# Kernel tuning notes

Measured on AMD Instinct MI355X. Metric: run time of the kernel, lower is better.

The kernel has to match this reference:

```python
import jax, jax.numpy as jnp
import numpy as np

N = 50000
E = 800000
NFEAT, NHID, NCLASS = 256, 128, 32


def setup_inputs() -> dict:
    key = jax.random.key(0)
    ks = jax.random.split(key, 8)
    x = jax.random.normal(ks[0], (N, NFEAT), dtype=jnp.float32)
    edge_src = jax.random.randint(ks[1], (E,), 0, N, dtype=jnp.int32)
    edge_dst = jax.random.randint(ks[2], (E,), 0, N, dtype=jnp.int32)
    edge_weight = jax.random.uniform(ks[3], (E,), dtype=jnp.float32)
    # Linear layer params (torch Linear: y = x @ W.T + b); store as [in, out]
    s1 = 1.0 / np.sqrt(NFEAT)
    s2 = 1.0 / np.sqrt(NHID)
    W1 = jax.random.uniform(ks[4], (NFEAT, NHID), jnp.float32, -s1, s1)
    b1 = jax.random.uniform(ks[5], (NHID,), jnp.float32, -s1, s1)
    W2 = jax.random.uniform(ks[6], (NHID, NCLASS), jnp.float32, -s2, s2)
    b2 = jax.random.uniform(ks[7], (NCLASS,), jnp.float32, -s2, s2)
    return {"x": x, "edge_src": edge_src, "edge_dst": edge_dst,
            "edge_weight": edge_weight, "W1": W1, "b1": b1, "W2": W2, "b2": b2}


def spmm(edge_src, edge_dst, edge_weight, h):
    # out[dst] += w * h[src]  -- sparse adjacency @ dense features
    msgs = edge_weight[:, None] * h[edge_src]          # [E, F]
    return jax.ops.segment_sum(msgs, edge_dst, num_segments=N)


def reference(x, edge_src, edge_dst, edge_weight, W1, b1, W2, b2):
    # GCN layer 1: Linear -> SpMM -> ReLU (dropout inactive in eval mode)
    h = x @ W1 + b1                                    # [N, NHID]
    h = spmm(edge_src, edge_dst, edge_weight, h)
    h = jax.nn.relu(h)
    # GCN layer 2: Linear -> SpMM
    h = h @ W2 + b2                                    # [N, NCLASS]
    out = spmm(edge_src, edge_dst, edge_weight, h)
    return out
```

## Files before the change

### kernel.cpp

```cpp
#include <hip/hip_runtime.h>

#define NFEAT 256
#define NHID 128
#define NCLASS 32

typedef __attribute__((ext_vector_type(8))) short short8;
typedef __attribute__((ext_vector_type(4))) float f32x4;
typedef __attribute__((ext_vector_type(4))) int int4v;

static __device__ __forceinline__ unsigned short f2bf(float f) {
    unsigned u = __float_as_uint(f);
    unsigned r = (u + 0x7fffu + ((u >> 16) & 1u)) >> 16;
    return (unsigned short)r;
}
static __device__ __forceinline__ float bf_lo(unsigned d) {
    return __uint_as_float(d << 16);
}
static __device__ __forceinline__ float bf_hi(unsigned d) {
    return __uint_as_float(d & 0xffff0000u);
}

__global__ __launch_bounds__(256) void prep_kernel(
    const float* __restrict__ W1, unsigned short* __restrict__ W1t,
    const int* __restrict__ dst, int* __restrict__ bkt_partial,
    int E, int CE, int shift)
{
    const int tid = threadIdx.x;
    if (blockIdx.x < 128) {
        int o = blockIdx.x * 256 + tid;
        int c = o >> 8, k = o & 255;
        W1t[o] = f2bf(W1[(size_t)k * NHID + c]);
    } else {
        __shared__ int h[256];
        const int kb = blockIdx.x - 128;
        const int start = kb * CE;
        const int end = min(start + CE, E);
        h[tid] = 0;
        __syncthreads();
        for (int e = start + tid; e < end; e += 256)
            atomicAdd(&h[dst[e] >> shift], 1);
        __syncthreads();
        bkt_partial[kb * 256 + tid] = h[tid];
    }
}

__global__ __launch_bounds__(256) void scan_kernel(
    const int* __restrict__ bkt_partial, int* __restrict__ chunk_pre,
    int* __restrict__ bkt_base, int E)
{
    __shared__ int s[256];
    const int t = threadIdx.x;
    int run = 0;
    for (int kb = 0; kb < 256; ++kb) {
        chunk_pre[kb * 256 + t] = run;
        run += bkt_partial[kb * 256 + t];
    }
    s[t] = run;
    __syncthreads();
    for (int off = 1; off < 256; off <<= 1) {
        int tv = (t >= off) ? s[t - off] : 0;
        __syncthreads();
        s[t] += tv;
        __syncthreads();
    }
    bkt_base[t] = s[t] - run;
    if (t == 255) bkt_base[256] = s[255];
}

__global__ __launch_bounds__(256) void bucket_scatter_kernel(
    const int* __restrict__ src, const int* __restrict__ dst,
    const float* __restrict__ w, const int* __restrict__ bkt_base,
    const int* __restrict__ chunk_pre, uint2* __restrict__ bkt_edges,
    int E, int CE, int shift)
{
    __shared__ int cur[256];
    const int tid = threadIdx.x;
    const int kb = blockIdx.x;
    cur[tid] = bkt_base[tid] + chunk_pre[kb * 256 + tid];
    __syncthreads();
    const int start = kb * CE;
    const int end = min(start + CE, E);
    const unsigned lmask = (1u << shift) - 1u;
    for (int e = start + tid; e < end; e += 256) {
        int d = dst[e];
        int b = d >> shift;
        int pos = atomicAdd(&cur[b], 1);
        uint2 rec;
        rec.x = (unsigned)src[e] | (((unsigned)d & lmask) << 24);
        rec.y = __float_as_uint(w[e]);
        bkt_edges[pos] = rec;
    }
}

__global__ __launch_bounds__(1024) void fine_scatter_kernel(
    const int* __restrict__ bkt_base, const uint2* __restrict__ bkt_edges,
    int* __restrict__ row_ptr, uint2* __restrict__ csr_e,
    int shift, int N, int E)
{
    __shared__ int h[256];
    __shared__ int cur[256];
    const int b = blockIdx.x;
    const int t = threadIdx.x;
    const int lo = bkt_base[b], hi = bkt_base[b + 1];
    const int dbase = b << shift;

    if (t < 256) h[t] = 0;
    __syncthreads();
    for (int i = lo + t; i < hi; i += 1024)
        atomicAdd(&h[bkt_edges[i].x >> 24], 1);
    __syncthreads();
    int v = (t < 256) ? h[t] : 0;
    for (int off = 1; off < 256; off <<= 1) {
        int tv = (t >= off && t < 256) ? h[t - off] : 0;
        __syncthreads();
        if (t < 256) h[t] += tv;
        __syncthreads();
    }
    if (t < 256) {
        int excl = h[t] - v;
        int r = dbase + t;
        if (r < N) row_ptr[r] = lo + excl;
        cur[t] = lo + excl;
    }
    if (b == 0 && t == 0) row_ptr[N] = E;
    __syncthreads();
    for (int i = lo + t; i < hi; i += 1024) {
        uint2 rec = bkt_edges[i];
        int dl = rec.x >> 24;
        int pos = atomicAdd(&cur[dl], 1);
        uint2 o;
        o.x = rec.x & 0xFFFFFFu;
        o.y = rec.y;
        csr_e[pos] = o;
    }
}

__global__ __launch_bounds__(256) void gemm1_mfma_kernel(
    const float* __restrict__ x, const unsigned short* __restrict__ W1t,
    const float* __restrict__ b1, unsigned short* __restrict__ h1b, int N)
{
    __shared__ unsigned short wt[128 * 256];
    __shared__ unsigned short xs[64 * 64];

    const int tid = threadIdx.x;
    const int lane = tid & 63;
    const int wv = tid >> 6;
    const int row0 = blockIdx.x * 64;
    const int l15 = lane & 15;
    const int l47 = lane >> 4;
    const int r7 = lane & 7;

    {
        const int4v* src = (const int4v*)W1t;
#pragma unroll
        for (int j = 0; j < 16; ++j) {
            int si = tid + j * 256;
            int c = si >> 5, s = si & 31;
            int sp = (s & 24) | ((s & 7) ^ (c & 7));
            int4v v = src[si];
            *(int4v*)&wt[c * 256 + sp * 8] = v;
        }
    }

    auto stage_x = [&](int t) {
#pragma unroll
        for (int j = 0; j < 2; ++j) {
            int si = tid + j * 256;
            int r = si >> 3, s = si & 7;
            int row = row0 + r;
            float4 v0 = make_float4(0.f, 0.f, 0.f, 0.f), v1 = v0;
            if (row < N) {
                const float4* xp = (const float4*)&x[(size_t)row * NFEAT + t * 64 + s * 8];
                v0 = xp[0]; v1 = xp[1];
            }
            int w0 = f2bf(v0.x) | ((unsigned)f2bf(v0.y) << 16);
            int w1 = f2bf(v0.z) | ((unsigned)f2bf(v0.w) << 16);
            int w2 = f2bf(v1.x) | ((unsigned)f2bf(v1.y) << 16);
            int w3 = f2bf(v1.z) | ((unsigned)f2bf(v1.w) << 16);
            int sp = s ^ (r & 7);
            int4v pv; pv[0] = w0; pv[1] = w1; pv[2] = w2; pv[3] = w3;
            *(int4v*)&xs[r * 64 + sp * 8] = pv;
        }
    };

    f32x4 acc[8];
#pragma unroll
    for (int cf = 0; cf < 8; ++cf)
#pragma unroll
        for (int r = 0; r < 4; ++r) acc[cf][r] = 0.f;

    stage_x(0);
    __syncthreads();

    const int arow = wv * 16 + l15;
#pragma unroll
    for (int t = 0; t < 4; ++t) {
        short8 af[2];
#pragma unroll
        for (int kf = 0; kf < 2; ++kf) {
            int slot = (kf * 4 + l47) ^ r7;
            af[kf] = *(const short8*)&xs[arow * 64 + slot * 8];
        }
#pragma unroll
        for (int cf = 0; cf < 8; ++cf) {
            const int brow = cf * 16 + l15;
#pragma unroll
            for (int kf = 0; kf < 2; ++kf) {
                int slot = t * 8 + ((kf * 4 + l47) ^ r7);
                short8 bfr = *(const short8*)&wt[brow * 256 + slot * 8];
                acc[cf] = __builtin_amdgcn_mfma_f32_16x16x32_bf16(af[kf], bfr, acc[cf], 0, 0, 0);
            }
        }
        __syncthreads();
        if (t < 3) {
            stage_x(t + 1);
            __syncthreads();
        }
    }

#pragma unroll
    for (int cf = 0; cf < 8; ++cf) {
        float bias = b1[cf * 16 + l15];
#pragma unroll
        for (int r = 0; r < 4; ++r) {
            int row = row0 + wv * 16 + l47 * 4 + r;
            if (row < N)
                h1b[(size_t)row * NHID + cf * 16 + l15] = f2bf(acc[cf][r] + bias);
        }
    }
}

__global__ __launch_bounds__(512) void spmm1_gemm2_kernel(
    const int* __restrict__ row_ptr, const uint2* __restrict__ csr_e,
    const unsigned short* __restrict__ h1b, const float* __restrict__ W2,
    const float* __restrict__ b2, unsigned* __restrict__ h2b, int N)
{
    __shared__ float w2s[NHID * NCLASS];
    __shared__ float hrow[8][NHID];
    const int tid = threadIdx.x;
#pragma unroll
    for (int j = 0; j < 8; ++j) {
        int idx = tid + j * 512;
        w2s[idx] = W2[idx];
    }
    __syncthreads();

    const int lane = tid & 63;
    const int wv = tid >> 6;
    const int row = __builtin_amdgcn_readfirstlane(blockIdx.x * 8 + wv);
    if (row >= N) return;

    const int e0 = row_ptr[row], e1 = row_ptr[row + 1];
    const size_t loff = (size_t)(lane * 2);
    float a0 = 0.f, a1 = 0.f;
    int e = e0;
    for (; e + 8 <= e1; e += 8) {
        uint2 r[8];
#pragma unroll
        for (int j = 0; j < 8; ++j) r[j] = csr_e[e + j];
        unsigned d[8];
#pragma unroll
        for (int j = 0; j < 8; ++j)
            d[j] = *(const unsigned*)(h1b + (size_t)r[j].x * NHID + loff);
#pragma unroll
        for (int j = 0; j < 8; ++j) {
            float w = __uint_as_float(r[j].y);
            a0 += w * bf_lo(d[j]); a1 += w * bf_hi(d[j]);
        }
    }
    if (e + 4 <= e1) {
        uint2 r[4];
#pragma unroll
        for (int j = 0; j < 4; ++j) r[j] = csr_e[e + j];
        unsigned d[4];
#pragma unroll
        for (int j = 0; j < 4; ++j)
            d[j] = *(const unsigned*)(h1b + (size_t)r[j].x * NHID + loff);
#pragma unroll
        for (int j = 0; j < 4; ++j) {
            float w = __uint_as_float(r[j].y);
            a0 += w * bf_lo(d[j]); a1 += w * bf_hi(d[j]);
        }
        e += 4;
    }
    if (e + 2 <= e1) {
        uint2 r0 = csr_e[e], r1 = csr_e[e + 1];
        unsigned d0 = *(const unsigned*)(h1b + (size_t)r0.x * NHID + loff);
        unsigned d1 = *(const unsigned*)(h1b + (size_t)r1.x * NHID + loff);
        float w0 = __uint_as_float(r0.y), w1 = __uint_as_float(r1.y);
        a0 += w0 * bf_lo(d0); a1 += w0 * bf_hi(d0);
        a0 += w1 * bf_lo(d1); a1 += w1 * bf_hi(d1);
        e += 2;
    }
    if (e < e1) {
        uint2 r = csr_e[e];
        float w = __uint_as_float(r.y);
        unsigned d = *(const unsigned*)(h1b + (size_t)r.x * NHID + loff);
        a0 += w * bf_lo(d); a1 += w * bf_hi(d);
    }
    *(float2*)&hrow[wv][lane * 2] = make_float2(fmaxf(a0, 0.f), fmaxf(a1, 0.f));

    const int c = lane & 31;
    const int kh = lane >> 5;
    const float* hw = &hrow[wv][kh * 64];
    const float* wp = &w2s[(size_t)kh * 64 * NCLASS + c];
    float acc = 0.f;
#pragma unroll
    for (int k = 0; k < 64; ++k)
        acc += hw[k] * wp[k * NCLASS];
    acc += __shfl(acc, lane ^ 32);
    float accb = acc + b2[c];
    float nb = __shfl(accb, lane ^ 1);
    if (kh == 0 && (lane & 1) == 0) {
        unsigned u = (unsigned)f2bf(accb) | ((unsigned)f2bf(nb) << 16);
        h2b[(size_t)row * 16 + (lane >> 1)] = u;
    }
}

__global__ __launch_bounds__(256) void spmm2_kernel(
    const int* __restrict__ row_ptr, const uint2* __restrict__ csr_e,
    const unsigned* __restrict__ h2b, float* __restrict__ out, int N)
{
    const int li = threadIdx.x & 15;
    const int g = threadIdx.x >> 4;
    const int row = blockIdx.x * 16 + g;
    if (row >= N) return;
    const int e0 = row_ptr[row], e1 = row_ptr[row + 1];
    float a0 = 0.f, a1 = 0.f;
    int e = e0;
    for (; e + 8 <= e1; e += 8) {
        uint2 r[8];
#pragma unroll
        for (int j = 0; j < 8; ++j) r[j] = csr_e[e + j];
        unsigned d[8];
#pragma unroll
        for (int j = 0; j < 8; ++j) d[j] = h2b[(size_t)r[j].x * 16 + li];
#pragma unroll
        for (int j = 0; j < 8; ++j) {
            float w = __uint_as_float(r[j].y);
            a0 += w * bf_lo(d[j]); a1 += w * bf_hi(d[j]);
        }
    }
    for (; e + 2 <= e1; e += 2) {
        uint2 r0 = csr_e[e], r1 = csr_e[e + 1];
        unsigned d0 = h2b[(size_t)r0.x * 16 + li];
        unsigned d1 = h2b[(size_t)r1.x * 16 + li];
        float w0 = __uint_as_float(r0.y), w1 = __uint_as_float(r1.y);
        a0 += w0 * bf_lo(d0); a1 += w0 * bf_hi(d0);
        a0 += w1 * bf_lo(d1); a1 += w1 * bf_hi(d1);
    }
    if (e < e1) {
        uint2 r = csr_e[e];
        float w = __uint_as_float(r.y);
        unsigned d = h2b[(size_t)r.x * 16 + li];
        a0 += w * bf_lo(d); a1 += w * bf_hi(d);
    }
    *(float2*)&out[(size_t)row * NCLASS + li * 2] = make_float2(a0, a1);
}


extern "C" void kernel_launch(void* const* d_in, const int* in_sizes, int n_in,
                              void* d_out, int out_size, void* d_ws, size_t ws_size,
                              hipStream_t stream) {
    const float* x    = (const float*)d_in[0];
    const int*   esrc = (const int*)d_in[1];
    const int*   edst = (const int*)d_in[2];
    const float* ew   = (const float*)d_in[3];
    const float* W1   = (const float*)d_in[4];
    const float* b1   = (const float*)d_in[5];
    const float* W2   = (const float*)d_in[6];
    const float* b2   = (const float*)d_in[7];
    float* out = (float*)d_out;

    const int N = in_sizes[0] / NFEAT;
    const int E = in_sizes[1];

    int shift = 0;
    while (((N - 1) >> shift) >= 256) ++shift;
    const int NBKT = ((N - 1) >> shift) + 1;
    const int CE = (E + 255) / 256;

    char* base = (char*)d_ws;
    size_t off = 0;
    auto take = [&](size_t bytes) -> void* {
        void* p = base + off;
        off += (bytes + 255) & ~(size_t)255;
        return p;
    };
    unsigned short* h1b = (unsigned short*)take((size_t)N * NHID * sizeof(unsigned short));
    unsigned* h2b  = (unsigned*)take((size_t)N * 16 * sizeof(unsigned));
    int*   row_ptr = (int*)take((size_t)(N + 1) * sizeof(int));
    int*   bkt_partial = (int*)take(256 * 256 * sizeof(int));
    int*   chunk_pre   = (int*)take(256 * 256 * sizeof(int));
    int*   bkt_base    = (int*)take(257 * sizeof(int));
    uint2* bkt_edges   = (uint2*)take((size_t)E * sizeof(uint2));
    uint2* csr_e       = (uint2*)take((size_t)E * sizeof(uint2));
    unsigned short* W1t = (unsigned short*)take((size_t)NFEAT * NHID * sizeof(unsigned short));
    (void)ws_size; (void)n_in; (void)out_size;

    prep_kernel<<<384, 256, 0, stream>>>(W1, W1t, edst, bkt_partial, E, CE, shift);
    scan_kernel<<<1, 256, 0, stream>>>(bkt_partial, chunk_pre, bkt_base, E);
    bucket_scatter_kernel<<<256, 256, 0, stream>>>(esrc, edst, ew, bkt_base, chunk_pre,
                                                   bkt_edges, E, CE, shift);
    fine_scatter_kernel<<<NBKT, 1024, 0, stream>>>(bkt_base, bkt_edges, row_ptr, csr_e,
                                                   shift, N, E);
    gemm1_mfma_kernel<<<(N + 63) / 64, 256, 0, stream>>>(x, W1t, b1, h1b, N);
    spmm1_gemm2_kernel<<<(N + 7) / 8, 512, 0, stream>>>(row_ptr, csr_e, h1b, W2, b2, h2b, N);
    spmm2_kernel<<<(N + 15) / 16, 256, 0, stream>>>(row_ptr, csr_e, h2b, out, N);
}
```

Baseline: 112.4 us.

## Vectorize edge loads, stream W1 tiles in GEMM1, unroll SpMM2 by 16

The histogram and bucket-scatter loops now read dst/src/w as int4/float4, with the chunk size rounded up to a multiple of 4 so the vector loads stay aligned. GEMM1 now stages a 64-wide K slice of W1t into LDS on each iteration instead of the full 64KB matrix, which cuts LDS use and should let more blocks fit per CU. The cost is reloading W1 slices every step and losing the overlap of x staging. SpMM2 gains a 16-edge unrolled loop that issues more gathers per iteration, at the cost of higher register pressure.

```diff
diff --git a/kernel.cpp b/kernel.cpp
--- a/kernel.cpp
+++ b/kernel.cpp
@@ -37,8 +37,18 @@
         const int end = min(start + CE, E);
         h[tid] = 0;
         __syncthreads();
-        for (int e = start + tid; e < end; e += 256)
-            atomicAdd(&h[dst[e] >> shift], 1);
+        for (int e4 = start + tid * 4; e4 < end; e4 += 1024) {
+            if (e4 + 3 < end) {
+                int4 d4 = *(const int4*)&dst[e4];
+                atomicAdd(&h[d4.x >> shift], 1);
+                atomicAdd(&h[d4.y >> shift], 1);
+                atomicAdd(&h[d4.z >> shift], 1);
+                atomicAdd(&h[d4.w >> shift], 1);
+            } else {
+                for (int e = e4; e < end; ++e)
+                    atomicAdd(&h[dst[e] >> shift], 1);
+            }
+        }
         __syncthreads();
         bkt_partial[kb * 256 + tid] = h[tid];
     }
@@ -81,14 +91,34 @@
     const int start = kb * CE;
     const int end = min(start + CE, E);
     const unsigned lmask = (1u << shift) - 1u;
-    for (int e = start + tid; e < end; e += 256) {
-        int d = dst[e];
-        int b = d >> shift;
-        int pos = atomicAdd(&cur[b], 1);
-        uint2 rec;
-        rec.x = (unsigned)src[e] | (((unsigned)d & lmask) << 24);
-        rec.y = __float_as_uint(w[e]);
-        bkt_edges[pos] = rec;
+    for (int e4 = start + tid * 4; e4 < end; e4 += 1024) {
+        if (e4 + 3 < end) {
+            int4 d4 = *(const int4*)&dst[e4];
+            int4 s4 = *(const int4*)&src[e4];
+            float4 w4 = *(const float4*)&w[e4];
+            int dd[4] = {d4.x, d4.y, d4.z, d4.w};
+            int ss[4] = {s4.x, s4.y, s4.z, s4.w};
+            float ww[4] = {w4.x, w4.y, w4.z, w4.w};
+#pragma unroll
+            for (int j = 0; j < 4; ++j) {
+                int b = dd[j] >> shift;
+                int pos = atomicAdd(&cur[b], 1);
+                uint2 rec;
+                rec.x = (unsigned)ss[j] | (((unsigned)dd[j] & lmask) << 24);
+                rec.y = __float_as_uint(ww[j]);
+                bkt_edges[pos] = rec;
+            }
+        } else {
+            for (int e = e4; e < end; ++e) {
+                int d = dst[e];
+                int b = d >> shift;
+                int pos = atomicAdd(&cur[b], 1);
+                uint2 rec;
+                rec.x = (unsigned)src[e] | (((unsigned)d & lmask) << 24);
+                rec.y = __float_as_uint(w[e]);
+                bkt_edges[pos] = rec;
+            }
+        }
     }
 }
 
@@ -139,7 +169,7 @@
     const float* __restrict__ x, const unsigned short* __restrict__ W1t,
     const float* __restrict__ b1, unsigned short* __restrict__ h1b, int N)
 {
-    __shared__ unsigned short wt[128 * 256];
+    __shared__ unsigned short wt[128 * 64];
     __shared__ unsigned short xs[64 * 64];
 
     const int tid = threadIdx.x;
@@ -150,18 +180,17 @@
     const int l47 = lane >> 4;
     const int r7 = lane & 7;
 
-    {
-        const int4v* src = (const int4v*)W1t;
-#pragma unroll
-        for (int j = 0; j < 16; ++j) {
+    auto stage_wt = [&](int t) {
+#pragma unroll
+        for (int j = 0; j < 4; ++j) {
             int si = tid + j * 256;
-            int c = si >> 5, s = si & 31;
-            int sp = (s & 24) | ((s & 7) ^ (c & 7));
-            int4v v = src[si];
-            *(int4v*)&wt[c * 256 + sp * 8] = v;
-        }
-    }
-
+            int c = si >> 3, s = si & 7;
+            int sp = s ^ (c & 7);
+            const int4v* wsrc = (const int4v*)(W1t + (size_t)c * 256 + t * 64);
+            int4v v = wsrc[s];
+            *(int4v*)&wt[c * 64 + sp * 8] = v;
+        }
+    };
     auto stage_x = [&](int t) {
 #pragma unroll
         for (int j = 0; j < 2; ++j) {
@@ -189,12 +218,12 @@
 #pragma unroll
         for (int r = 0; r < 4; ++r) acc[cf][r] = 0.f;
 
-    stage_x(0);
-    __syncthreads();
-
     const int arow = wv * 16 + l15;
 #pragma unroll
     for (int t = 0; t < 4; ++t) {
+        stage_wt(t);
+        stage_x(t);
+        __syncthreads();
         short8 af[2];
 #pragma unroll
         for (int kf = 0; kf < 2; ++kf) {
@@ -206,16 +235,12 @@
             const int brow = cf * 16 + l15;
 #pragma unroll
             for (int kf = 0; kf < 2; ++kf) {
-                int slot = t * 8 + ((kf * 4 + l47) ^ r7);
-                short8 bfr = *(const short8*)&wt[brow * 256 + slot * 8];
+                int slot = (kf * 4 + l47) ^ r7;
+                short8 bfr = *(const short8*)&wt[brow * 64 + slot * 8];
                 acc[cf] = __builtin_amdgcn_mfma_f32_16x16x32_bf16(af[kf], bfr, acc[cf], 0, 0, 0);
             }
         }
         __syncthreads();
-        if (t < 3) {
-            stage_x(t + 1);
-            __syncthreads();
-        }
     }
 
 #pragma unroll
@@ -328,6 +353,19 @@
     const int e0 = row_ptr[row], e1 = row_ptr[row + 1];
     float a0 = 0.f, a1 = 0.f;
     int e = e0;
+    for (; e + 16 <= e1; e += 16) {
+        uint2 r[16];
+#pragma unroll
+        for (int j = 0; j < 16; ++j) r[j] = csr_e[e + j];
+        unsigned d[16];
+#pragma unroll
+        for (int j = 0; j < 16; ++j) d[j] = h2b[(size_t)r[j].x * 16 + li];
+#pragma unroll
+        for (int j = 0; j < 16; ++j) {
+            float w = __uint_as_float(r[j].y);
+            a0 += w * bf_lo(d[j]); a1 += w * bf_hi(d[j]);
+        }
+    }
     for (; e + 8 <= e1; e += 8) {
         uint2 r[8];
 #pragma unroll
@@ -378,7 +416,7 @@
     int shift = 0;
     while (((N - 1) >> shift) >= 256) ++shift;
     const int NBKT = ((N - 1) >> shift) + 1;
-    const int CE = (E + 255) / 256;
+    const int CE = (((E + 255) / 256) + 3) & ~3;
 
     char* base = (char*)d_ws;
     size_t off = 0;
```

Measured after the change: 102.7 us, median of 2. 8.6% less time.
